# Performance work log

Hardware: AMD Instinct MI355X
Metric: run time of the kernel (lower is better)

Reference implementation:

```python
import jax, jax.numpy as jnp
import numpy as np

TOP_K = 2

def setup_inputs() -> dict:
    key = jax.random.key(0)
    k1, k2 = jax.random.split(key)
    G, S, D, E = 4, 2048, 2048, 64
    x = jax.random.normal(k1, (G, S, D), dtype=jnp.float32)
    # xavier_normal-ish scale for the gate kernel
    W = jax.random.normal(k2, (D, E), dtype=jnp.float32) * (2.0 / (D + E)) ** 0.5
    b = jnp.zeros((E,), dtype=jnp.float32)
    return {"x": x, "W": W, "b": b, "expert_capacity": 64}

def reference(x, W, b, expert_capacity):
    # gate projection: [G,S,D] @ [D,E] -> [G,S,E]
    gating_logits = jnp.einsum('gsd,de->gse', x, W) + b
    gating_probs = jax.nn.softmax(gating_logits, axis=-1)
    # top-k experts per token
    expert_gate, expert_index = jax.lax.top_k(gating_probs, TOP_K)  # [G,S,K]
    E = gating_probs.shape[2]
    expert_mask = jax.nn.one_hot(expert_index, E)  # [G,S,K,E]
    # position of each token within its chosen expert (1-based for selected slots)
    position_in_expert = jnp.cumsum(expert_mask, axis=1) * expert_mask  # [G,S,K,E]
    valid_assignment = position_in_expert < expert_capacity
    expert_gate_valid = expert_gate[..., None] * valid_assignment.astype(expert_gate.dtype)
    # one-hot over capacity slots: [G,S,K,E,C]
    combine_per_assignment = expert_gate_valid[..., None] * jax.nn.one_hot(
        position_in_expert, expert_capacity)
    combine_tensor = jnp.sum(combine_per_assignment, axis=2)  # [G,S,E,C]
    combine_tensor = combine_tensor[..., 1:]  # drop position-0 slot -> [G,S,E,C-1]
    dispatch_mask = combine_tensor.astype(bool)
    loss = 0.0  # training=False path
    return combine_tensor, dispatch_mask, loss
```

## Files before the change

kernel.cpp:

```cpp
#include <hip/hip_runtime.h>
#include <cstdint>
#include <cstddef>

#define G_    4
#define S_    2048
#define D_    2048
#define E_    64
#define NTOK  (G_ * S_)
#define CAPM1 63
#define COMBINE_SZ ((size_t)NTOK * E_ * CAPM1)
#define KSLICES 4
#define KCHUNK  (D_ / KSLICES)

__global__ __launch_bounds__(256) void gemm_partial_k(
    const float* __restrict__ x, const float* __restrict__ W,
    float* __restrict__ partial)
{
    __shared__ float xs[16][64];
    __shared__ float wls[16][64];

    const int tid     = threadIdx.x;
    const int tokBase = blockIdx.x * 64;
    const int kBase   = blockIdx.y * KCHUNK;

    const int tt = (tid >> 4) << 2;
    const int ee = (tid & 15) << 2;

    const int xrow = tid >> 2;
    const int xkq  = (tid & 3) << 2;
    const int wkr  = tid >> 4;
    const int wec  = (tid & 15) << 2;

    float acc[4][4];
#pragma unroll
    for (int i = 0; i < 4; ++i)
#pragma unroll
        for (int j = 0; j < 4; ++j) acc[i][j] = 0.f;

    for (int kc = 0; kc < KCHUNK; kc += 16) {
        const float4 xv = *reinterpret_cast<const float4*>(
            &x[(size_t)(tokBase + xrow) * D_ + (size_t)(kBase + kc + xkq)]);
        const float4 wv = *reinterpret_cast<const float4*>(
            &W[(size_t)(kBase + kc + wkr) * E_ + wec]);
        __syncthreads();
        xs[xkq + 0][xrow] = xv.x;
        xs[xkq + 1][xrow] = xv.y;
        xs[xkq + 2][xrow] = xv.z;
        xs[xkq + 3][xrow] = xv.w;
        *reinterpret_cast<float4*>(&wls[wkr][wec]) = wv;
        __syncthreads();
#pragma unroll
        for (int k = 0; k < 16; ++k) {
            const float4 xa = *reinterpret_cast<const float4*>(&xs[k][tt]);
            const float4 wb = *reinterpret_cast<const float4*>(&wls[k][ee]);
            acc[0][0] += xa.x * wb.x; acc[0][1] += xa.x * wb.y;
            acc[0][2] += xa.x * wb.z; acc[0][3] += xa.x * wb.w;
            acc[1][0] += xa.y * wb.x; acc[1][1] += xa.y * wb.y;
            acc[1][2] += xa.y * wb.z; acc[1][3] += xa.y * wb.w;
            acc[2][0] += xa.z * wb.x; acc[2][1] += xa.z * wb.y;
            acc[2][2] += xa.z * wb.z; acc[2][3] += xa.z * wb.w;
            acc[3][0] += xa.w * wb.x; acc[3][1] += xa.w * wb.y;
            acc[3][2] += xa.w * wb.z; acc[3][3] += xa.w * wb.w;
        }
    }

    float* dst = partial + (size_t)blockIdx.y * ((size_t)NTOK * E_);
#pragma unroll
    for (int i = 0; i < 4; ++i) {
        float4 v = make_float4(acc[i][0], acc[i][1], acc[i][2], acc[i][3]);
        *reinterpret_cast<float4*>(&dst[(size_t)(tokBase + tt + i) * E_ + ee]) = v;
    }
}

__global__ __launch_bounds__(256) void softmax_top2_k(
    const float* __restrict__ partial, const float* __restrict__ b,
    int* __restrict__ e1, int* __restrict__ e2,
    float* __restrict__ g1, float* __restrict__ g2)
{
    const int lane = threadIdx.x & 63;
    const int w    = threadIdx.x >> 6;
    const int tok  = blockIdx.x * 4 + w;

    float v = b[lane];
#pragma unroll
    for (int sl = 0; sl < KSLICES; ++sl)
        v += partial[(size_t)sl * NTOK * E_ + (size_t)tok * E_ + lane];

    float m = v;
#pragma unroll
    for (int off = 32; off >= 1; off >>= 1) m = fmaxf(m, __shfl_xor(m, off));
    float p = expf(v - m);
    float s = p;
#pragma unroll
    for (int off = 32; off >= 1; off >>= 1) s += __shfl_xor(s, off);
    p = p / s;

    float bp = p; int bi = lane;
#pragma unroll
    for (int off = 32; off >= 1; off >>= 1) {
        float po = __shfl_xor(bp, off);
        int   io = __shfl_xor(bi, off);
        if (po > bp || (po == bp && io < bi)) { bp = po; bi = io; }
    }
    float p2 = (lane == bi) ? -1.0f : p;
    float bp2 = p2; int bi2 = lane;
#pragma unroll
    for (int off = 32; off >= 1; off >>= 1) {
        float po = __shfl_xor(bp2, off);
        int   io = __shfl_xor(bi2, off);
        if (po > bp2 || (po == bp2 && io < bi2)) { bp2 = po; bi2 = io; }
    }

    if (lane == 0) {
        e1[tok] = bi;  e2[tok] = bi2;
        g1[tok] = bp;  g2[tok] = bp2;
    }
}

__global__ __launch_bounds__(1024) void route_scatter_k(
    const int* __restrict__ e1, const int* __restrict__ e2,
    const float* __restrict__ g1, const float* __restrict__ g2,
    float* __restrict__ out)
{
    __shared__ int cnt[2][32][64];

    const int g    = blockIdx.x;
    const int lane = threadIdx.x & 63;
    const int wid  = threadIdx.x >> 6;
    const unsigned long long ltmask = ((unsigned long long)1 << lane) - 1;

    int myE[2][2];
    int rank[2][2];

#pragma unroll
    for (int seg = 0; seg < 2; ++seg) {
        const int wseg = seg * 16 + wid;
        const int tok  = g * S_ + wseg * 64 + lane;
        const int ea = e1[tok];
        const int eb = e2[tok];
        myE[seg][0] = ea;
        myE[seg][1] = eb;
#pragma unroll
        for (int k = 0; k < 2; ++k) {
            const int me = k ? eb : ea;
            int r = 0;
            for (int e = 0; e < 64; ++e) {
                unsigned long long mask = __ballot(me == e);
                if (lane == e) cnt[k][wseg][e] = __popcll(mask);
                if (me == e)   r = __popcll(mask & ltmask);
            }
            rank[seg][k] = r;
        }
    }
    __syncthreads();

    if (threadIdx.x < 128) {
        const int k = threadIdx.x >> 6;
        const int e = threadIdx.x & 63;
        int run = 0;
        for (int w = 0; w < 32; ++w) {
            int c = cnt[k][w][e];
            cnt[k][w][e] = run;
            run += c;
        }
    }
    __syncthreads();

#pragma unroll
    for (int seg = 0; seg < 2; ++seg) {
        const int wseg = seg * 16 + wid;
        const int tok  = g * S_ + wseg * 64 + lane;
#pragma unroll
        for (int k = 0; k < 2; ++k) {
            const int e   = myE[seg][k];
            const int pos = cnt[k][wseg][e] + rank[seg][k] + 1;
            if (pos <= CAPM1) {
                const float gate = k ? g2[tok] : g1[tok];
                const size_t idx = ((size_t)tok * E_ + e) * CAPM1 + (pos - 1);
                out[idx] = gate;
                out[idx + COMBINE_SZ] = 1.0f;
            }
        }
    }
}

extern "C" void kernel_launch(void* const* d_in, const int* in_sizes, int n_in,
                              void* d_out, int out_size, void* d_ws, size_t ws_size,
                              hipStream_t stream)
{
    const float* x = (const float*)d_in[0];
    const float* W = (const float*)d_in[1];
    const float* b = (const float*)d_in[2];
    float* out = (float*)d_out;

    float* partial = (float*)d_out;

    int*   e1 = (int*)d_ws;
    int*   e2 = e1 + NTOK;
    float* g1 = (float*)(e2 + NTOK);
    float* g2 = g1 + NTOK;

    gemm_partial_k<<<dim3(NTOK / 64, KSLICES), 256, 0, stream>>>(x, W, partial);
    softmax_top2_k<<<NTOK / 4, 256, 0, stream>>>(partial, b, e1, e2, g1, g2);
    hipMemsetAsync(d_out, 0, (size_t)out_size * sizeof(float), stream);
    route_scatter_k<<<G_, 1024, 0, stream>>>(e1, e2, g1, g2, out);
}
```

Before: 382.3 us.

## Replace memset plus scatter with a single dense output writer kernel

Instead of zero-filling the whole output with a memset and then scattering gate values, the routing kernel now stores per-token expert, slot and gate records, and a new grid-stride kernel writes every output element once as a float4 (zero or the value). This removes the separate memset pass and the random scattered writes over the large output. The K split of the gate GEMM also goes from 4 to 8 slices to expose more parallelism. The writer recomputes row and column with a magic-multiply divide and rereads small per-token records for each vector it writes.

```diff
diff --git a/kernel.cpp b/kernel.cpp
--- a/kernel.cpp
+++ b/kernel.cpp
@@ -9,7 +9,7 @@
 #define NTOK  (G_ * S_)
 #define CAPM1 63
 #define COMBINE_SZ ((size_t)NTOK * E_ * CAPM1)
-#define KSLICES 4
+#define KSLICES 8
 #define KCHUNK  (D_ / KSLICES)
 
 __global__ __launch_bounds__(256) void gemm_partial_k(
@@ -117,9 +117,10 @@
     }
 }
 
-__global__ __launch_bounds__(1024) void route_scatter_k(
+__global__ __launch_bounds__(1024) void route_pos_k(
     const int* __restrict__ e1, const int* __restrict__ e2,
     const float* __restrict__ g1, const float* __restrict__ g2,
+    int4* __restrict__ recI, float2* __restrict__ recF,
     float* __restrict__ out)
 {
     __shared__ int cnt[2][32][64];
@@ -170,17 +171,61 @@
     for (int seg = 0; seg < 2; ++seg) {
         const int wseg = seg * 16 + wid;
         const int tok  = g * S_ + wseg * 64 + lane;
+        int pm1[2];
 #pragma unroll
         for (int k = 0; k < 2; ++k) {
             const int e   = myE[seg][k];
             const int pos = cnt[k][wseg][e] + rank[seg][k] + 1;
-            if (pos <= CAPM1) {
-                const float gate = k ? g2[tok] : g1[tok];
-                const size_t idx = ((size_t)tok * E_ + e) * CAPM1 + (pos - 1);
-                out[idx] = gate;
-                out[idx + COMBINE_SZ] = 1.0f;
+            pm1[k] = (pos <= CAPM1) ? (pos - 1) : -1;
+        }
+        recI[tok] = make_int4(myE[seg][0], myE[seg][1], pm1[0], pm1[1]);
+        recF[tok] = make_float2(g1[tok], g2[tok]);
+    }
+
+    if (g == 0 && threadIdx.x == 0) out[2 * COMBINE_SZ] = 0.0f;
+}
+
+__global__ __launch_bounds__(256) void write_all_k(
+    const int4* __restrict__ recI, const float2* __restrict__ recF,
+    float* __restrict__ out)
+{
+    const size_t nvec = (2 * COMBINE_SZ) / 4;
+    const size_t stride = (size_t)gridDim.x * blockDim.x;
+
+    for (size_t i = (size_t)blockIdx.x * blockDim.x + threadIdx.x;
+         i < nvec; i += stride) {
+        const size_t f = i * 4;
+        const bool isMask = f >= COMBINE_SZ;
+        uint32_t fm = (uint32_t)(isMask ? f - COMBINE_SZ : f);
+
+        uint32_t row = (uint32_t)(((uint64_t)fm * 272696337ULL) >> 34);
+        uint32_t c   = fm - row * 63u;
+
+        uint32_t e = row & 63u, tok = row >> 6;
+        int4   ri = recI[tok];
+        float2 rf = recF[tok];
+        int c1 = (e == (uint32_t)ri.x) ? ri.z : -1;
+        int c2 = (e == (uint32_t)ri.y) ? ri.w : -1;
+        float v1 = isMask ? 1.0f : rf.x;
+        float v2 = isMask ? 1.0f : rf.y;
+
+        float4 v;
+        float* vp = &v.x;
+#pragma unroll
+        for (int j = 0; j < 4; ++j) {
+            if (c == 63u) {
+                c = 0; ++row;
+                e = row & 63u; tok = row >> 6;
+                ri = recI[tok]; rf = recF[tok];
+                c1 = (e == (uint32_t)ri.x) ? ri.z : -1;
+                c2 = (e == (uint32_t)ri.y) ? ri.w : -1;
+                v1 = isMask ? 1.0f : rf.x;
+                v2 = isMask ? 1.0f : rf.y;
             }
-        }
+            vp[j] = ((int)c == c1) ? v1 : ((int)c == c2) ? v2 : 0.0f;
+            ++c;
+        }
+        *reinterpret_cast<float4*>(&out[f]) = v;
     }
 }
 
@@ -195,13 +240,15 @@
 
     float* partial = (float*)d_out;
 
-    int*   e1 = (int*)d_ws;
-    int*   e2 = e1 + NTOK;
-    float* g1 = (float*)(e2 + NTOK);
-    float* g2 = g1 + NTOK;
+    int*    e1   = (int*)d_ws;
+    int*    e2   = e1 + NTOK;
+    float*  g1   = (float*)(e2 + NTOK);
+    float*  g2   = g1 + NTOK;
+    int4*   recI = (int4*)(g2 + NTOK);
+    float2* recF = (float2*)(recI + NTOK);
 
     gemm_partial_k<<<dim3(NTOK / 64, KSLICES), 256, 0, stream>>>(x, W, partial);
     softmax_top2_k<<<NTOK / 4, 256, 0, stream>>>(partial, b, e1, e2, g1, g2);
-    hipMemsetAsync(d_out, 0, (size_t)out_size * sizeof(float), stream);
-    route_scatter_k<<<G_, 1024, 0, stream>>>(e1, e2, g1, g2, out);
-}
+    route_pos_k<<<G_, 1024, 0, stream>>>(e1, e2, g1, g2, recI, recF, out);
+    write_all_k<<<2048, 256, 0, stream>>>(recI, recF, out);
+}
```

New measurement: 396.5 us. +3.7%, slower.
